# Performance work log

Hardware: AMD Instinct MI355X
Metric: run time of the kernel (lower is better)

The kernel has to match this reference:

```python
import jax, jax.numpy as jnp
import numpy as np

N_NODES = 50000


def setup_inputs() -> dict:
    key = jax.random.key(0)
    ks = jax.random.split(key, 9)
    d = 256
    E = 800000
    inp = {
        "x": jax.random.normal(ks[0], (N_NODES, d), dtype=jnp.float32),
        "edge_index": jax.random.randint(ks[1], (2, E), 0, N_NODES, dtype=jnp.int64),
    }
    # 3 GCNConv layers, each: weight [in, out] and bias [out] (Glorot-ish scale)
    scale = 1.0 / np.sqrt(d)
    for i in range(3):
        inp[f"W{i+1}"] = jax.random.normal(ks[2 + 2 * i], (d, d), dtype=jnp.float32) * scale
        inp[f"b{i+1}"] = jnp.zeros((d,), dtype=jnp.float32)
    return inp


def _gcn_conv(h, src, dst, norm, W, b, n_nodes):
    # linear transform then normalized gather-scatter aggregation
    h = h @ W                                   # [N, out]
    msg = h[src] * norm[:, None]                # [E+N, out]
    out = jax.ops.segment_sum(msg, dst, num_segments=n_nodes)
    return out + b


def reference(x, edge_index, W1, b1, W2, b2, W3, b3):
    n = x.shape[0]
    loop = jnp.arange(n, dtype=edge_index.dtype)
    src = jnp.concatenate([edge_index[0], loop])  # add self-loops
    dst = jnp.concatenate([edge_index[1], loop])
    # symmetric normalization: deg^{-1/2}[src] * deg^{-1/2}[dst]
    deg = jax.ops.segment_sum(jnp.ones_like(dst, dtype=x.dtype), dst, num_segments=n)
    dinv = jnp.where(deg > 0, jax.lax.rsqrt(deg), 0.0)
    norm = dinv[src] * dinv[dst]

    h = _gcn_conv(x, src, dst, norm, W1, b1, n)
    h = jax.nn.relu(h)
    h = _gcn_conv(h, src, dst, norm, W2, b2, n)
    h = jax.nn.relu(h)
    h = _gcn_conv(h, src, dst, norm, W3, b3, n)
    return h
```

## Files before the change

kernel.cpp:

```cpp
#include <hip/hip_runtime.h>
#include <math.h>


using f16x8   = __attribute__((ext_vector_type(8))) _Float16;
using ushort4v = __attribute__((ext_vector_type(4))) unsigned short;
using f32x4   = __attribute__((ext_vector_type(4))) float;
using half4   = __attribute__((ext_vector_type(4))) _Float16;

__device__ inline unsigned short f2h_bits(float v) {
    _Float16 h = (_Float16)v;
    union { _Float16 h; unsigned short u; } c; c.h = h;
    return c.u;
}


__global__ void hist_kernel(const int* __restrict__ dst, int E, int* __restrict__ cnt) {
    int e = blockIdx.x * blockDim.x + threadIdx.x;
    if (e < E) atomicAdd(&cnt[dst[e]], 1);
}

__global__ void scan_block_kernel(const int* __restrict__ in, int n,
                                  int* __restrict__ out, int* __restrict__ bsums) {
    __shared__ int s[256];
    int t = threadIdx.x;
    int i = blockIdx.x * 256 + t;
    s[t] = (i < n) ? in[i] : 0;
    __syncthreads();
    for (int off = 1; off < 256; off <<= 1) {
        int addv = (t >= off) ? s[t - off] : 0;
        __syncthreads();
        s[t] += addv;
        __syncthreads();
    }
    if (i < n) out[i] = s[t];
    if (t == 255) bsums[blockIdx.x] = s[255];
}

__global__ void scan_sums_kernel(int* __restrict__ bsums, int nb) {
    __shared__ int s[256];
    int t = threadIdx.x;
    s[t] = (t < nb) ? bsums[t] : 0;
    __syncthreads();
    for (int off = 1; off < 256; off <<= 1) {
        int addv = (t >= off) ? s[t - off] : 0;
        __syncthreads();
        s[t] += addv;
        __syncthreads();
    }
    if (t < nb) bsums[t] = s[t];
}

__global__ void scan_add_dinv_kernel(int* __restrict__ scn, int n, const int* __restrict__ bsums,
                                     const int* __restrict__ cnt, float* __restrict__ dinv,
                                     int* __restrict__ cursor) {
    int i = blockIdx.x * 256 + threadIdx.x;
    if (i < n) {
        int s = scn[i] + (blockIdx.x > 0 ? bsums[blockIdx.x - 1] : 0);
        scn[i] = s;
        int c = cnt[i];
        dinv[i] = rsqrtf((float)(c + 1));
        cursor[i] = s - c;
    }
}

__global__ void scatter_kernel(const int* __restrict__ src, const int* __restrict__ dst, int E,
                               const float* __restrict__ dinv, int* __restrict__ cursor,
                               int* __restrict__ ssrc, float* __restrict__ snorm) {
    int e = blockIdx.x * blockDim.x + threadIdx.x;
    if (e < E) {
        int s = src[e], d0 = dst[e];
        int pos = atomicAdd(&cursor[d0], 1);
        ssrc[pos] = s;
        snorm[pos] = dinv[s] * dinv[d0];
    }
}

__global__ __launch_bounds__(256) void wsplit3_kernel(const float* __restrict__ Wa,
                                                      const float* __restrict__ Wb,
                                                      const float* __restrict__ Wc,
                                                      unsigned short* __restrict__ Wsp) {
    __shared__ float t[64][65];
    int w = blockIdx.z;
    const float* W = (w == 0) ? Wa : (w == 1) ? Wb : Wc;
    int k0 = blockIdx.x * 64, n0 = blockIdx.y * 64;
    int tid = threadIdx.x;
    int r = tid >> 6, c = tid & 63;
#pragma unroll
    for (int i = 0; i < 16; ++i) {
        int kk = i * 4 + r;
        t[kk][c] = W[(size_t)(k0 + kk) * 256 + n0 + c];
    }
    __syncthreads();
    unsigned short* Hi = Wsp + (size_t)w * 131072;
    unsigned short* Lo = Hi + 65536;
#pragma unroll
    for (int i = 0; i < 16; ++i) {
        int nn = i * 4 + r;
        float v = t[c][nn];
        _Float16 hh = (_Float16)v;
        float rr = v - (float)hh;
        _Float16 ll = (_Float16)rr;
        union { _Float16 h; unsigned short u; } ch, cl; ch.h = hh; cl.h = ll;
        Hi[(size_t)(n0 + nn) * 256 + k0 + c] = ch.u;
        Lo[(size_t)(n0 + nn) * 256 + k0 + c] = cl.u;
    }
}

__global__ void xcast_kernel(const float* __restrict__ in, unsigned short* __restrict__ out16,
                             int total4) {
    int i = blockIdx.x * blockDim.x + threadIdx.x;
    int stride = gridDim.x * blockDim.x;
    for (; i < total4; i += stride) {
        float4 v = ((const float4*)in)[i];
        ushort4v o;
        o[0] = f2h_bits(v.x); o[1] = f2h_bits(v.y);
        o[2] = f2h_bits(v.z); o[3] = f2h_bits(v.w);
        ((ushort4v*)out16)[i] = o;
    }
}

__global__ __launch_bounds__(512) void gemm_f16_kernel(
        const unsigned short* __restrict__ Af, const unsigned short* __restrict__ Whf,
        const unsigned short* __restrict__ Wlf, unsigned short* __restrict__ C16, int M) {
    __shared__ unsigned short lds[40960];

    const int tid  = threadIdx.x;
    const int lane = tid & 63;
    const int wid  = tid >> 6;
    const int wr   = wid >> 2;
    const int wc   = wid & 3;
    const int mBase = blockIdx.x * 128;

    const int b0 = (lane ^ (lane >> 2) ^ (lane >> 4)) & 1;
    const int b1 = ((lane >> 1) ^ (lane >> 3)) & 1;
    const int b2 = ((lane >> 2) ^ (lane >> 4)) & 1;
    const int g  = (lane & 0x38) | (b2 << 2) | (b1 << 1) | b0;
    const int srow = g >> 2;
    const int skg  = g & 3;

    const unsigned short* cptr[5];
    int cdst[5];
#pragma unroll
    for (int i = 0; i < 5; ++i) {
        int c = wid * 5 + i;
        const unsigned short* base;
        int row, dst;
        if (c < 8) {
            base = Af;
            row = mBase + c * 16 + srow;
            if (row >= M) row = M - 1;
            dst = c * 512;
        } else if (c < 24) {
            base = Whf;
            row = (c - 8) * 16 + srow;
            dst = 4096 + (c - 8) * 512;
        } else {
            base = Wlf;
            row = (c - 24) * 16 + srow;
            dst = 12288 + (c - 24) * 512;
        }
        cptr[i] = base + (size_t)row * 256 + skg * 8;
        cdst[i] = dst;
    }

    f32x4 acc[4][4];
#pragma unroll
    for (int i = 0; i < 4; ++i)
#pragma unroll
        for (int j = 0; j < 4; ++j) acc[i][j] = (f32x4){0.f, 0.f, 0.f, 0.f};

    auto stage = [&](int p, int k) {
        unsigned short* dbase = lds + p * 20480;
        const int k0 = k * 32;
#pragma unroll
        for (int i = 0; i < 5; ++i) {
            __builtin_amdgcn_global_load_lds(
                (const __attribute__((address_space(1))) void*)(cptr[i] + k0),
                (__attribute__((address_space(3))) void*)(dbase + cdst[i]),
                16, 0, 0);
        }
    };

    stage(0, 0);

#pragma unroll
    for (int k = 0; k < 8; ++k) {
        const int p = k & 1;
        if (k < 7) {
            stage(p ^ 1, k + 1);
            asm volatile("s_waitcnt vmcnt(5)" ::: "memory");
        } else {
            asm volatile("s_waitcnt vmcnt(0)" ::: "memory");
        }
        __builtin_amdgcn_s_barrier();

        const unsigned short* As = lds + p * 20480;
        const unsigned short* Bh = As + 4096;
        const unsigned short* Bl = As + 12288;

        const int kb = (lane >> 4) * 8;
        f16x8 fa[4], fbh[4], fbl[4];
#pragma unroll
        for (int mi = 0; mi < 4; ++mi) {
            int row = wr * 64 + mi * 16 + (lane & 15);
            int off = (row * 64 + kb * 2) ^ ((row & 7) << 4);
            fa[mi] = *(const f16x8*)((const char*)As + off);
        }
#pragma unroll
        for (int ni = 0; ni < 4; ++ni) {
            int col = wc * 64 + ni * 16 + (lane & 15);
            int off = (col * 64 + kb * 2) ^ ((col & 7) << 4);
            fbh[ni] = *(const f16x8*)((const char*)Bh + off);
            fbl[ni] = *(const f16x8*)((const char*)Bl + off);
        }
#pragma unroll
        for (int mi = 0; mi < 4; ++mi)
#pragma unroll
            for (int ni = 0; ni < 4; ++ni) {
                acc[mi][ni] = __builtin_amdgcn_mfma_f32_16x16x32_f16(
                    fa[mi], fbh[ni], acc[mi][ni], 0, 0, 0);
                acc[mi][ni] = __builtin_amdgcn_mfma_f32_16x16x32_f16(
                    fa[mi], fbl[ni], acc[mi][ni], 0, 0, 0);
            }
        __builtin_amdgcn_s_barrier();
    }

#pragma unroll
    for (int mi = 0; mi < 4; ++mi) {
        int row0 = mBase + wr * 64 + mi * 16 + (lane >> 4) * 4;
#pragma unroll
        for (int ni = 0; ni < 4; ++ni) {
            int col = wc * 64 + ni * 16 + (lane & 15);
#pragma unroll
            for (int r = 0; r < 4; ++r) {
                int row = row0 + r;
                if (row < M) C16[(size_t)row * 256 + col] = f2h_bits(acc[mi][ni][r]);
            }
        }
    }
}

template <int RELU, int SPLIT>
__global__ __launch_bounds__(256) void agg_kernel(const unsigned short* __restrict__ hH,
                                                  const int* __restrict__ ssrc,
                                                  const float* __restrict__ snorm,
                                                  const int* __restrict__ cnt,
                                                  const int* __restrict__ scanv,
                                                  const float* __restrict__ dinv,
                                                  const float* __restrict__ bias,
                                                  unsigned short* __restrict__ outH,
                                                  float* __restrict__ outF, int n) {
    int node = blockIdx.x * 4 + (threadIdx.x >> 6);
    int lane = threadIdx.x & 63;
    if (node >= n) return;
    int end = scanv[node];
    int start = end - cnt[node];
    float di = dinv[node];
    float wself = di * di;

    half4 v = ((const half4*)(hH + (size_t)node * 256))[lane];
    float ax = (float)v[0] * wself, ay = (float)v[1] * wself;
    float az = (float)v[2] * wself, aw = (float)v[3] * wself;

    int j = start;
    for (; j + 4 <= end; j += 4) {
        int s0 = ssrc[j], s1 = ssrc[j + 1], s2 = ssrc[j + 2], s3 = ssrc[j + 3];
        float w0 = snorm[j], w1 = snorm[j + 1], w2 = snorm[j + 2], w3 = snorm[j + 3];
        half4 u0 = ((const half4*)(hH + (size_t)s0 * 256))[lane];
        half4 u1 = ((const half4*)(hH + (size_t)s1 * 256))[lane];
        half4 u2 = ((const half4*)(hH + (size_t)s2 * 256))[lane];
        half4 u3 = ((const half4*)(hH + (size_t)s3 * 256))[lane];
        ax = fmaf((float)u0[0], w0, ax); ay = fmaf((float)u0[1], w0, ay);
        az = fmaf((float)u0[2], w0, az); aw = fmaf((float)u0[3], w0, aw);
        ax = fmaf((float)u1[0], w1, ax); ay = fmaf((float)u1[1], w1, ay);
        az = fmaf((float)u1[2], w1, az); aw = fmaf((float)u1[3], w1, aw);
        ax = fmaf((float)u2[0], w2, ax); ay = fmaf((float)u2[1], w2, ay);
        az = fmaf((float)u2[2], w2, az); aw = fmaf((float)u2[3], w2, aw);
        ax = fmaf((float)u3[0], w3, ax); ay = fmaf((float)u3[1], w3, ay);
        az = fmaf((float)u3[2], w3, az); aw = fmaf((float)u3[3], w3, aw);
    }
    for (; j < end; ++j) {
        int s = ssrc[j];
        float wn = snorm[j];
        half4 u = ((const half4*)(hH + (size_t)s * 256))[lane];
        ax = fmaf((float)u[0], wn, ax); ay = fmaf((float)u[1], wn, ay);
        az = fmaf((float)u[2], wn, az); aw = fmaf((float)u[3], wn, aw);
    }

    float4 bb = ((const float4*)bias)[lane];
    ax += bb.x; ay += bb.y; az += bb.z; aw += bb.w;
    if (RELU) {
        ax = fmaxf(ax, 0.0f); ay = fmaxf(ay, 0.0f);
        az = fmaxf(az, 0.0f); aw = fmaxf(aw, 0.0f);
    }
    if (SPLIT) {
        ushort4v o;
        o[0] = f2h_bits(ax); o[1] = f2h_bits(ay);
        o[2] = f2h_bits(az); o[3] = f2h_bits(aw);
        ((ushort4v*)(outH + (size_t)node * 256))[lane] = o;
    } else {
        float4 o = {ax, ay, az, aw};
        ((float4*)(outF + (size_t)node * 256))[lane] = o;
    }
}

extern "C" void kernel_launch(void* const* d_in, const int* in_sizes, int n_in,
                              void* d_out, int out_size, void* d_ws, size_t ws_size,
                              hipStream_t stream) {
    const float* x  = (const float*)d_in[0];
    const int*   ei = (const int*)d_in[1];
    const float* W1 = (const float*)d_in[2];
    const float* b1 = (const float*)d_in[3];
    const float* W2 = (const float*)d_in[4];
    const float* b2 = (const float*)d_in[5];
    const float* W3 = (const float*)d_in[6];
    const float* b3 = (const float*)d_in[7];

    const int n = in_sizes[0] / 256;
    const int E = in_sizes[1] / 2;
    const int* src = ei;
    const int* dst = ei + E;

    unsigned short* hAct = (unsigned short*)d_out;
    unsigned short* xF   = hAct + (size_t)n * 256;
    float* outF = (float*)d_out;

    char* ws = (char*)d_ws;
    unsigned short* hLin = (unsigned short*)ws;
    size_t off  = (size_t)n * 256 * 2;
    off = (off + 255) & ~(size_t)255;
    float* dinv = (float*)(ws + off); off += (size_t)n * 4;
    int*   cnt  = (int*)(ws + off);   off += (size_t)n * 4;
    int*   scn  = (int*)(ws + off);   off += (size_t)n * 4;
    int*   cur  = (int*)(ws + off);   off += (size_t)n * 4;
    int*   bsum = (int*)(ws + off);   off += 4096;
    int*   ssrc = (int*)(ws + off);   off += (size_t)E * 4;
    float* snrm = (float*)(ws + off); off += (size_t)E * 4;
    off = (off + 255) & ~(size_t)255;
    unsigned short* Wsp = (unsigned short*)(ws + off);
    off += (size_t)3 * 2 * 65536 * 2;

    hipMemsetAsync(cnt, 0, (size_t)n * 4, stream);

    const int eb = (E + 255) / 256;
    const int nb = (n + 255) / 256;

    wsplit3_kernel<<<dim3(4, 4, 3), 256, 0, stream>>>(W1, W2, W3, Wsp);
    xcast_kernel<<<2048, 256, 0, stream>>>(x, xF, n * 64);

    hist_kernel<<<eb, 256, 0, stream>>>(dst, E, cnt);
    scan_block_kernel<<<nb, 256, 0, stream>>>(cnt, n, scn, bsum);
    scan_sums_kernel<<<1, 256, 0, stream>>>(bsum, nb);
    scan_add_dinv_kernel<<<nb, 256, 0, stream>>>(scn, n, bsum, cnt, dinv, cur);
    scatter_kernel<<<eb, 256, 0, stream>>>(src, dst, E, dinv, cur, ssrc, snrm);

    const int gb = (n + 127) / 128;
    const int ab = (n + 3) / 4;

    gemm_f16_kernel<<<gb, 512, 0, stream>>>(xF, Wsp, Wsp + 65536, hLin, n);
    agg_kernel<1, 1><<<ab, 256, 0, stream>>>(hLin, ssrc, snrm, cnt, scn, dinv, b1,
                                             hAct, nullptr, n);
    gemm_f16_kernel<<<gb, 512, 0, stream>>>(hAct, Wsp + 131072, Wsp + 196608, hLin, n);
    agg_kernel<1, 1><<<ab, 256, 0, stream>>>(hLin, ssrc, snrm, cnt, scn, dinv, b2,
                                             hAct, nullptr, n);
    gemm_f16_kernel<<<gb, 512, 0, stream>>>(hAct, Wsp + 262144, Wsp + 327680, hLin, n);
    agg_kernel<0, 0><<<ab, 256, 0, stream>>>(hLin, ssrc, snrm, cnt, scn, dinv, b3,
                                             nullptr, outF, n);
}
```

Baseline: 359.9 us.

## Fuse aggregation with following layer GEMM via LDS-resident activation tile

```diff
diff --git a/kernel.cpp b/kernel.cpp
--- a/kernel.cpp
+++ b/kernel.cpp
@@ -240,6 +240,168 @@
     }
 }
 
+__global__ __launch_bounds__(512) void fused_agg_gemm_kernel(
+        const unsigned short* __restrict__ hH,
+        const int* __restrict__ ssrc, const float* __restrict__ snorm,
+        const int* __restrict__ cnt, const int* __restrict__ scanv,
+        const float* __restrict__ dinv, const float* __restrict__ bias,
+        const unsigned short* __restrict__ Whf, const unsigned short* __restrict__ Wlf,
+        unsigned short* __restrict__ C16, int n) {
+    __shared__ unsigned short lds[65536];
+
+    const int tid  = threadIdx.x;
+    const int lane = tid & 63;
+    const int wid  = tid >> 6;
+    const int mBase = blockIdx.x * 128;
+
+    for (int i = 0; i < 16; ++i) {
+        const int r = wid * 16 + i;
+        const int node = mBase + r;
+        float ax = 0.f, ay = 0.f, az = 0.f, aw = 0.f;
+        if (node < n) {
+            int end = scanv[node];
+            int start = end - cnt[node];
+            float di = dinv[node];
+            float wself = di * di;
+            half4 v = ((const half4*)(hH + (size_t)node * 256))[lane];
+            ax = (float)v[0] * wself; ay = (float)v[1] * wself;
+            az = (float)v[2] * wself; aw = (float)v[3] * wself;
+            int j = start;
+            for (; j + 4 <= end; j += 4) {
+                int s0 = ssrc[j], s1 = ssrc[j + 1], s2 = ssrc[j + 2], s3 = ssrc[j + 3];
+                float w0 = snorm[j], w1 = snorm[j + 1], w2 = snorm[j + 2], w3 = snorm[j + 3];
+                half4 u0 = ((const half4*)(hH + (size_t)s0 * 256))[lane];
+                half4 u1 = ((const half4*)(hH + (size_t)s1 * 256))[lane];
+                half4 u2 = ((const half4*)(hH + (size_t)s2 * 256))[lane];
+                half4 u3 = ((const half4*)(hH + (size_t)s3 * 256))[lane];
+                ax = fmaf((float)u0[0], w0, ax); ay = fmaf((float)u0[1], w0, ay);
+                az = fmaf((float)u0[2], w0, az); aw = fmaf((float)u0[3], w0, aw);
+                ax = fmaf((float)u1[0], w1, ax); ay = fmaf((float)u1[1], w1, ay);
+                az = fmaf((float)u1[2], w1, az); aw = fmaf((float)u1[3], w1, aw);
+                ax = fmaf((float)u2[0], w2, ax); ay = fmaf((float)u2[1], w2, ay);
+                az = fmaf((float)u2[2], w2, az); aw = fmaf((float)u2[3], w2, aw);
+                ax = fmaf((float)u3[0], w3, ax); ay = fmaf((float)u3[1], w3, ay);
+                az = fmaf((float)u3[2], w3, az); aw = fmaf((float)u3[3], w3, aw);
+            }
+            for (; j < end; ++j) {
+                int s = ssrc[j];
+                float wn = snorm[j];
+                half4 u = ((const half4*)(hH + (size_t)s * 256))[lane];
+                ax = fmaf((float)u[0], wn, ax); ay = fmaf((float)u[1], wn, ay);
+                az = fmaf((float)u[2], wn, az); aw = fmaf((float)u[3], wn, aw);
+            }
+            float4 bb = ((const float4*)bias)[lane];
+            ax += bb.x; ay += bb.y; az += bb.z; aw += bb.w;
+            ax = fmaxf(ax, 0.0f); ay = fmaxf(ay, 0.0f);
+            az = fmaxf(az, 0.0f); aw = fmaxf(aw, 0.0f);
+        }
+        ushort4v o;
+        o[0] = f2h_bits(ax); o[1] = f2h_bits(ay);
+        o[2] = f2h_bits(az); o[3] = f2h_bits(aw);
+        const int offA = r * 512 + ((lane * 8) ^ ((r & 7) << 4));
+        *(ushort4v*)((char*)lds + offA) = o;
+    }
+    __syncthreads();
+
+    const int wr = wid >> 2;
+    const int wc = wid & 3;
+
+    const int b0 = (lane ^ (lane >> 2) ^ (lane >> 4)) & 1;
+    const int b1 = ((lane >> 1) ^ (lane >> 3)) & 1;
+    const int b2 = ((lane >> 2) ^ (lane >> 4)) & 1;
+    const int g  = (lane & 0x38) | (b2 << 2) | (b1 << 1) | b0;
+    const int srow = g >> 2;
+    const int skg  = g & 3;
+
+    const unsigned short* cptr[4];
+    int crel[4];
+#pragma unroll
+    for (int i = 0; i < 4; ++i) {
+        int c = wid * 4 + i;
+        const unsigned short* base = (c < 16) ? Whf : Wlf;
+        int cc = (c < 16) ? c : c - 16;
+        int row = cc * 16 + srow;
+        cptr[i] = base + (size_t)row * 256 + skg * 8;
+        crel[i] = (c < 16 ? 0 : 8192) + cc * 512;
+    }
+
+    f32x4 acc[4][4];
+#pragma unroll
+    for (int i = 0; i < 4; ++i)
+#pragma unroll
+        for (int j = 0; j < 4; ++j) acc[i][j] = (f32x4){0.f, 0.f, 0.f, 0.f};
+
+    auto stage = [&](int p, int k) {
+        unsigned short* dbase = lds + 32768 + p * 16384;
+        const int k0 = k * 32;
+#pragma unroll
+        for (int i = 0; i < 4; ++i) {
+            __builtin_amdgcn_global_load_lds(
+                (const __attribute__((address_space(1))) void*)(cptr[i] + k0),
+                (__attribute__((address_space(3))) void*)(dbase + crel[i]),
+                16, 0, 0);
+        }
+    };
+
+    stage(0, 0);
+
+#pragma unroll
+    for (int k = 0; k < 8; ++k) {
+        const int p = k & 1;
+        if (k < 7) {
+            stage(p ^ 1, k + 1);
+            asm volatile("s_waitcnt vmcnt(4)" ::: "memory");
+        } else {
+            asm volatile("s_waitcnt vmcnt(0)" ::: "memory");
+        }
+        __builtin_amdgcn_s_barrier();
+
+        const unsigned short* WhL = lds + 32768 + p * 16384;
+        const unsigned short* WlL = WhL + 8192;
+
+        const int kb = (lane >> 4) * 8;
+        const int colb = k * 64 + (lane >> 4) * 16;
+        f16x8 fa[4], fbh[4], fbl[4];
+#pragma unroll
+        for (int mi = 0; mi < 4; ++mi) {
+            int row = wr * 64 + mi * 16 + (lane & 15);
+            int offA = row * 512 + (colb ^ ((row & 7) << 4));
+            fa[mi] = *(const f16x8*)((const char*)lds + offA);
+        }
+#pragma unroll
+        for (int ni = 0; ni < 4; ++ni) {
+            int col = wc * 64 + ni * 16 + (lane & 15);
+            int offW = (col * 64 + kb * 2) ^ ((col & 7) << 4);
+            fbh[ni] = *(const f16x8*)((const char*)WhL + offW);
+            fbl[ni] = *(const f16x8*)((const char*)WlL + offW);
+        }
+#pragma unroll
+        for (int mi = 0; mi < 4; ++mi)
+#pragma unroll
+            for (int ni = 0; ni < 4; ++ni) {
+                acc[mi][ni] = __builtin_amdgcn_mfma_f32_16x16x32_f16(
+                    fa[mi], fbh[ni], acc[mi][ni], 0, 0, 0);
+                acc[mi][ni] = __builtin_amdgcn_mfma_f32_16x16x32_f16(
+                    fa[mi], fbl[ni], acc[mi][ni], 0, 0, 0);
+            }
+        __builtin_amdgcn_s_barrier();
+    }
+
+#pragma unroll
+    for (int mi = 0; mi < 4; ++mi) {
+        int row0 = mBase + wr * 64 + mi * 16 + (lane >> 4) * 4;
+#pragma unroll
+        for (int ni = 0; ni < 4; ++ni) {
+            int col = wc * 64 + ni * 16 + (lane & 15);
+#pragma unroll
+            for (int r = 0; r < 4; ++r) {
+                int row = row0 + r;
+                if (row < n) C16[(size_t)row * 256 + col] = f2h_bits(acc[mi][ni][r]);
+            }
+        }
+    }
+}
+
 template <int RELU, int SPLIT>
 __global__ __launch_bounds__(256) void agg_kernel(const unsigned short* __restrict__ hH,
                                                   const int* __restrict__ ssrc,
@@ -321,8 +483,8 @@
     const int* src = ei;
     const int* dst = ei + E;
 
-    unsigned short* hAct = (unsigned short*)d_out;
-    unsigned short* xF   = hAct + (size_t)n * 256;
+    unsigned short* hB = (unsigned short*)d_out;
+    unsigned short* xF = hB + (size_t)n * 256;
     float* outF = (float*)d_out;
 
     char* ws = (char*)d_ws;
@@ -358,12 +520,10 @@
     const int ab = (n + 3) / 4;
 
     gemm_f16_kernel<<<gb, 512, 0, stream>>>(xF, Wsp, Wsp + 65536, hLin, n);
-    agg_kernel<1, 1><<<ab, 256, 0, stream>>>(hLin, ssrc, snrm, cnt, scn, dinv, b1,
-                                             hAct, nullptr, n);
-    gemm_f16_kernel<<<gb, 512, 0, stream>>>(hAct, Wsp + 131072, Wsp + 196608, hLin, n);
-    agg_kernel<1, 1><<<ab, 256, 0, stream>>>(hLin, ssrc, snrm, cnt, scn, dinv, b2,
-                                             hAct, nullptr, n);
-    gemm_f16_kernel<<<gb, 512, 0, stream>>>(hAct, Wsp + 262144, Wsp + 327680, hLin, n);
+    fused_agg_gemm_kernel<<<gb, 512, 0, stream>>>(hLin, ssrc, snrm, cnt, scn, dinv, b1,
+                                                  Wsp + 131072, Wsp + 196608, hB, n);
+    fused_agg_gemm_kernel<<<gb, 512, 0, stream>>>(hB, ssrc, snrm, cnt, scn, dinv, b2,
+                                                  Wsp + 262144, Wsp + 327680, hLin, n);
     agg_kernel<0, 0><<<ab, 256, 0, stream>>>(hLin, ssrc, snrm, cnt, scn, dinv, b3,
                                              nullptr, outF, n);
 }
```

Measured after the change: 522.4 us. +45.2%, slower.

## Store node features in 8 column-slice planes for cache-local aggregation

Applied to the files above, without the earlier changes.

```diff
diff --git a/kernel.cpp b/kernel.cpp
--- a/kernel.cpp
+++ b/kernel.cpp
@@ -5,7 +5,6 @@
 using f16x8   = __attribute__((ext_vector_type(8))) _Float16;
 using ushort4v = __attribute__((ext_vector_type(4))) unsigned short;
 using f32x4   = __attribute__((ext_vector_type(4))) float;
-using half4   = __attribute__((ext_vector_type(4))) _Float16;
 
 __device__ inline unsigned short f2h_bits(float v) {
     _Float16 h = (_Float16)v;
@@ -106,8 +105,8 @@
     }
 }
 
-__global__ void xcast_kernel(const float* __restrict__ in, unsigned short* __restrict__ out16,
-                             int total4) {
+__global__ void xcast8_kernel(const float* __restrict__ in, unsigned short* __restrict__ out16,
+                              int n, int total4) {
     int i = blockIdx.x * blockDim.x + threadIdx.x;
     int stride = gridDim.x * blockDim.x;
     for (; i < total4; i += stride) {
@@ -115,7 +114,10 @@
         ushort4v o;
         o[0] = f2h_bits(v.x); o[1] = f2h_bits(v.y);
         o[2] = f2h_bits(v.z); o[3] = f2h_bits(v.w);
-        ((ushort4v*)out16)[i] = o;
+        int nd = i >> 6;
+        int f  = (i & 63) * 4;
+        size_t off = (size_t)(f >> 5) * n * 32 + (size_t)nd * 32 + (f & 31);
+        *(ushort4v*)(out16 + off) = o;
     }
 }
 
@@ -139,28 +141,28 @@
     const int skg  = g & 3;
 
     const unsigned short* cptr[5];
+    size_t kmul[5];
     int cdst[5];
 #pragma unroll
     for (int i = 0; i < 5; ++i) {
         int c = wid * 5 + i;
-        const unsigned short* base;
-        int row, dst;
         if (c < 8) {
-            base = Af;
-            row = mBase + c * 16 + srow;
+            int row = mBase + c * 16 + srow;
             if (row >= M) row = M - 1;
-            dst = c * 512;
+            cptr[i] = Af + (size_t)row * 32 + skg * 8;
+            kmul[i] = (size_t)M * 32;
+            cdst[i] = c * 512;
         } else if (c < 24) {
-            base = Whf;
-            row = (c - 8) * 16 + srow;
-            dst = 4096 + (c - 8) * 512;
+            int row = (c - 8) * 16 + srow;
+            cptr[i] = Whf + (size_t)row * 256 + skg * 8;
+            kmul[i] = 32;
+            cdst[i] = 4096 + (c - 8) * 512;
         } else {
-            base = Wlf;
-            row = (c - 24) * 16 + srow;
-            dst = 12288 + (c - 24) * 512;
-        }
-        cptr[i] = base + (size_t)row * 256 + skg * 8;
-        cdst[i] = dst;
+            int row = (c - 24) * 16 + srow;
+            cptr[i] = Wlf + (size_t)row * 256 + skg * 8;
+            kmul[i] = 32;
+            cdst[i] = 12288 + (c - 24) * 512;
+        }
     }
 
     f32x4 acc[4][4];
@@ -171,11 +173,10 @@
 
     auto stage = [&](int p, int k) {
         unsigned short* dbase = lds + p * 20480;
-        const int k0 = k * 32;
 #pragma unroll
         for (int i = 0; i < 5; ++i) {
             __builtin_amdgcn_global_load_lds(
-                (const __attribute__((address_space(1))) void*)(cptr[i] + k0),
+                (const __attribute__((address_space(1))) void*)(cptr[i] + (size_t)k * kmul[i]),
                 (__attribute__((address_space(3))) void*)(dbase + cdst[i]),
                 16, 0, 0);
         }
@@ -231,76 +232,68 @@
 #pragma unroll
         for (int ni = 0; ni < 4; ++ni) {
             int col = wc * 64 + ni * 16 + (lane & 15);
+            size_t sbase = (size_t)(col >> 5) * M * 32 + (col & 31);
 #pragma unroll
             for (int r = 0; r < 4; ++r) {
                 int row = row0 + r;
-                if (row < M) C16[(size_t)row * 256 + col] = f2h_bits(acc[mi][ni][r]);
+                if (row < M) C16[sbase + (size_t)row * 32] = f2h_bits(acc[mi][ni][r]);
             }
         }
     }
 }
 
 template <int RELU, int SPLIT>
-__global__ __launch_bounds__(256) void agg_kernel(const unsigned short* __restrict__ hH,
-                                                  const int* __restrict__ ssrc,
-                                                  const float* __restrict__ snorm,
-                                                  const int* __restrict__ cnt,
-                                                  const int* __restrict__ scanv,
-                                                  const float* __restrict__ dinv,
-                                                  const float* __restrict__ bias,
-                                                  unsigned short* __restrict__ outH,
-                                                  float* __restrict__ outF, int n) {
-    int node = blockIdx.x * 4 + (threadIdx.x >> 6);
-    int lane = threadIdx.x & 63;
+__global__ __launch_bounds__(256) void agg8_kernel(const unsigned short* __restrict__ hH,
+                                                   const int* __restrict__ ssrc,
+                                                   const float* __restrict__ snorm,
+                                                   const int* __restrict__ cnt,
+                                                   const int* __restrict__ scanv,
+                                                   const float* __restrict__ dinv,
+                                                   const float* __restrict__ bias,
+                                                   unsigned short* __restrict__ outH,
+                                                   float* __restrict__ outF, int n) {
+    const int slice = blockIdx.x & 7;
+    const int quad  = blockIdx.x >> 3;
+    const int tid   = threadIdx.x;
+    const int node  = quad * 8 + (tid >> 6) * 2 + ((tid >> 5) & 1);
+    const int l32   = tid & 31;
     if (node >= n) return;
+
+    const _Float16* hf = (const _Float16*)hH;
+    const size_t sbase = (size_t)slice * n * 32;
+
     int end = scanv[node];
     int start = end - cnt[node];
     float di = dinv[node];
     float wself = di * di;
 
-    half4 v = ((const half4*)(hH + (size_t)node * 256))[lane];
-    float ax = (float)v[0] * wself, ay = (float)v[1] * wself;
-    float az = (float)v[2] * wself, aw = (float)v[3] * wself;
+    float acc = (float)hf[sbase + (size_t)node * 32 + l32] * wself;
 
     int j = start;
     for (; j + 4 <= end; j += 4) {
         int s0 = ssrc[j], s1 = ssrc[j + 1], s2 = ssrc[j + 2], s3 = ssrc[j + 3];
         float w0 = snorm[j], w1 = snorm[j + 1], w2 = snorm[j + 2], w3 = snorm[j + 3];
-        half4 u0 = ((const half4*)(hH + (size_t)s0 * 256))[lane];
-        half4 u1 = ((const half4*)(hH + (size_t)s1 * 256))[lane];
-        half4 u2 = ((const half4*)(hH + (size_t)s2 * 256))[lane];
-        half4 u3 = ((const half4*)(hH + (size_t)s3 * 256))[lane];
-        ax = fmaf((float)u0[0], w0, ax); ay = fmaf((float)u0[1], w0, ay);
-        az = fmaf((float)u0[2], w0, az); aw = fmaf((float)u0[3], w0, aw);
-        ax = fmaf((float)u1[0], w1, ax); ay = fmaf((float)u1[1], w1, ay);
-        az = fmaf((float)u1[2], w1, az); aw = fmaf((float)u1[3], w1, aw);
-        ax = fmaf((float)u2[0], w2, ax); ay = fmaf((float)u2[1], w2, ay);
-        az = fmaf((float)u2[2], w2, az); aw = fmaf((float)u2[3], w2, aw);
-        ax = fmaf((float)u3[0], w3, ax); ay = fmaf((float)u3[1], w3, ay);
-        az = fmaf((float)u3[2], w3, az); aw = fmaf((float)u3[3], w3, aw);
+        float u0 = (float)hf[sbase + (size_t)s0 * 32 + l32];
+        float u1 = (float)hf[sbase + (size_t)s1 * 32 + l32];
+        float u2 = (float)hf[sbase + (size_t)s2 * 32 + l32];
+        float u3 = (float)hf[sbase + (size_t)s3 * 32 + l32];
+        acc = fmaf(u0, w0, acc);
+        acc = fmaf(u1, w1, acc);
+        acc = fmaf(u2, w2, acc);
+        acc = fmaf(u3, w3, acc);
     }
     for (; j < end; ++j) {
         int s = ssrc[j];
         float wn = snorm[j];
-        half4 u = ((const half4*)(hH + (size_t)s * 256))[lane];
-        ax = fmaf((float)u[0], wn, ax); ay = fmaf((float)u[1], wn, ay);
-        az = fmaf((float)u[2], wn, az); aw = fmaf((float)u[3], wn, aw);
-    }
-
-    float4 bb = ((const float4*)bias)[lane];
-    ax += bb.x; ay += bb.y; az += bb.z; aw += bb.w;
-    if (RELU) {
-        ax = fmaxf(ax, 0.0f); ay = fmaxf(ay, 0.0f);
-        az = fmaxf(az, 0.0f); aw = fmaxf(aw, 0.0f);
-    }
+        acc = fmaf((float)hf[sbase + (size_t)s * 32 + l32], wn, acc);
+    }
+
+    acc += bias[slice * 32 + l32];
+    if (RELU) acc = fmaxf(acc, 0.0f);
     if (SPLIT) {
-        ushort4v o;
-        o[0] = f2h_bits(ax); o[1] = f2h_bits(ay);
-        o[2] = f2h_bits(az); o[3] = f2h_bits(aw);
-        ((ushort4v*)(outH + (size_t)node * 256))[lane] = o;
+        outH[sbase + (size_t)node * 32 + l32] = f2h_bits(acc);
     } else {
-        float4 o = {ax, ay, az, aw};
-        ((float4*)(outF + (size_t)node * 256))[lane] = o;
+        outF[(size_t)node * 256 + slice * 32 + l32] = acc;
     }
 }
 
@@ -346,7 +339,7 @@
     const int nb = (n + 255) / 256;
 
     wsplit3_kernel<<<dim3(4, 4, 3), 256, 0, stream>>>(W1, W2, W3, Wsp);
-    xcast_kernel<<<2048, 256, 0, stream>>>(x, xF, n * 64);
+    xcast8_kernel<<<2048, 256, 0, stream>>>(x, xF, n, n * 64);
 
     hist_kernel<<<eb, 256, 0, stream>>>(dst, E, cnt);
     scan_block_kernel<<<nb, 256, 0, stream>>>(cnt, n, scn, bsum);
@@ -355,15 +348,15 @@
     scatter_kernel<<<eb, 256, 0, stream>>>(src, dst, E, dinv, cur, ssrc, snrm);
 
     const int gb = (n + 127) / 128;
-    const int ab = (n + 3) / 4;
+    const int ag = ((n + 7) / 8) * 8;
 
     gemm_f16_kernel<<<gb, 512, 0, stream>>>(xF, Wsp, Wsp + 65536, hLin, n);
-    agg_kernel<1, 1><<<ab, 256, 0, stream>>>(hLin, ssrc, snrm, cnt, scn, dinv, b1,
-                                             hAct, nullptr, n);
+    agg8_kernel<1, 1><<<ag, 256, 0, stream>>>(hLin, ssrc, snrm, cnt, scn, dinv, b1,
+                                              hAct, nullptr, n);
     gemm_f16_kernel<<<gb, 512, 0, stream>>>(hAct, Wsp + 131072, Wsp + 196608, hLin, n);
-    agg_kernel<1, 1><<<ab, 256, 0, stream>>>(hLin, ssrc, snrm, cnt, scn, dinv, b2,
-                                             hAct, nullptr, n);
+    agg8_kernel<1, 1><<<ag, 256, 0, stream>>>(hLin, ssrc, snrm, cnt, scn, dinv, b2,
+                                              hAct, nullptr, n);
     gemm_f16_kernel<<<gb, 512, 0, stream>>>(hAct, Wsp + 262144, Wsp + 327680, hLin, n);
-    agg_kernel<0, 0><<<ab, 256, 0, stream>>>(hLin, ssrc, snrm, cnt, scn, dinv, b3,
-                                             nullptr, outF, n);
-}
+    agg8_kernel<0, 0><<<ag, 256, 0, stream>>>(hLin, ssrc, snrm, cnt, scn, dinv, b3,
+                                              nullptr, outF, n);
+}
```

New measurement: 565.9 us. 1.57x slower.
